# Optimization experiments

Hardware: AMD Instinct MI355X
Metric: run time of the kernel (lower is better)

## Reference

```python
import jax, jax.numpy as jnp
import numpy as np

TAU = 2.0
V_THRESHOLD = 1.0
V_RESET = 0.0

def setup_inputs() -> dict:
    key = jax.random.key(0)
    x = jax.random.normal(key, (4, 64, 262144), dtype=jnp.float32)
    return {"x": x}

def reference(x) -> jnp.ndarray:
    # MultiStepLIFNodePTT with decay_input=False, hard reset to v_reset=0.
    # Per step: v = v + x_t - (v - v_reset)/tau ; s = H(v - thresh) ; v = v*(1-s) + v_reset*s
    T = x.shape[0]
    flat = x.reshape(T, -1)  # [T, B*N]
    v0 = jnp.zeros_like(flat[0])

    def step(v, x_t):
        v = v + x_t - (v - V_RESET) * (1.0 / TAU)
        s = (v >= V_THRESHOLD).astype(v.dtype)
        v = v * (1.0 - s) + V_RESET * s
        return v, s

    _, spike_seq = jax.lax.scan(step, v0, flat)
    return spike_seq.reshape(x.shape)
```

## Files before the change

kernel.cpp:

```cpp
#include <hip/hip_runtime.h>


#define T_STEPS 4

typedef float vf4 __attribute__((ext_vector_type(4)));

__device__ __forceinline__ vf4 lif_step(vf4& v, const vf4 xt)
{
    v = 0.5f * v + xt;
    vf4 s;
    s.x = (v.x >= 1.0f) ? 1.0f : 0.0f;
    s.y = (v.y >= 1.0f) ? 1.0f : 0.0f;
    s.z = (v.z >= 1.0f) ? 1.0f : 0.0f;
    s.w = (v.w >= 1.0f) ? 1.0f : 0.0f;
    v.x = (v.x >= 1.0f) ? 0.0f : v.x;
    v.y = (v.y >= 1.0f) ? 0.0f : v.y;
    v.z = (v.z >= 1.0f) ? 0.0f : v.z;
    v.w = (v.w >= 1.0f) ? 0.0f : v.w;
    return s;
}

__global__ __launch_bounds__(256) void lif_spike_kernel(
    const vf4* __restrict__ x, vf4* __restrict__ out, unsigned n4)
{
    const unsigned S   = gridDim.x * blockDim.x;
    const unsigned tid = blockIdx.x * blockDim.x + threadIdx.x;

    if (tid + 3u * S < n4) {
        vf4 xv[4][T_STEPS];
#pragma unroll
        for (int k = 0; k < 4; ++k) {
            const unsigned i = tid + (unsigned)k * S;
#pragma unroll
            for (int t = 0; t < T_STEPS; ++t)
                xv[k][t] = __builtin_nontemporal_load(&x[(size_t)t * n4 + i]);
        }
#pragma unroll
        for (int k = 0; k < 4; ++k) {
            const unsigned i = tid + (unsigned)k * S;
            vf4 v = (vf4)(0.f);
#pragma unroll
            for (int t = 0; t < T_STEPS; ++t) {
                const vf4 s = lif_step(v, xv[k][t]);
                __builtin_nontemporal_store(s, &out[(size_t)t * n4 + i]);
            }
        }
    } else {
        for (unsigned i = tid; i < n4; i += S) {
            const vf4 x0 = __builtin_nontemporal_load(&x[(size_t)0 * n4 + i]);
            const vf4 x1 = __builtin_nontemporal_load(&x[(size_t)1 * n4 + i]);
            const vf4 x2 = __builtin_nontemporal_load(&x[(size_t)2 * n4 + i]);
            const vf4 x3 = __builtin_nontemporal_load(&x[(size_t)3 * n4 + i]);
            vf4 v = (vf4)(0.f);
            const vf4 s0 = lif_step(v, x0);
            const vf4 s1 = lif_step(v, x1);
            const vf4 s2 = lif_step(v, x2);
            const vf4 s3 = lif_step(v, x3);
            __builtin_nontemporal_store(s0, &out[(size_t)0 * n4 + i]);
            __builtin_nontemporal_store(s1, &out[(size_t)1 * n4 + i]);
            __builtin_nontemporal_store(s2, &out[(size_t)2 * n4 + i]);
            __builtin_nontemporal_store(s3, &out[(size_t)3 * n4 + i]);
        }
    }
}

extern "C" void kernel_launch(void* const* d_in, const int* in_sizes, int n_in,
                              void* d_out, int out_size, void* d_ws, size_t ws_size,
                              hipStream_t stream)
{
    const float* x = (const float*)d_in[0];
    float* out = (float*)d_out;

    const int n_total = in_sizes[0];
    const unsigned n4 = (unsigned)(n_total / T_STEPS / 4);

    const int block = 256;
    int grid = (int)(n4 / (unsigned)(block * 4));
    if (grid < 1) grid = 1;
    if ((unsigned)grid * (unsigned)block * 4u != n4) {
        grid = (int)((n4 + block - 1) / block);
        if (grid > 4096) grid = 4096;
    }

    lif_spike_kernel<<<grid, block, 0, stream>>>(
        (const vf4*)x, (vf4*)out, n4);
}
```

Before: 433.4 us.

## Simplify LIF kernel to fixed-grid grid-stride loop with regular stores

```diff
diff --git a/kernel.cpp b/kernel.cpp
--- a/kernel.cpp
+++ b/kernel.cpp
@@ -20,47 +20,26 @@
     return s;
 }
 
-__global__ __launch_bounds__(256) void lif_spike_kernel(
+__global__ __launch_bounds__(256, 8) void lif_spike_kernel(
     const vf4* __restrict__ x, vf4* __restrict__ out, unsigned n4)
 {
-    const unsigned S   = gridDim.x * blockDim.x;
-    const unsigned tid = blockIdx.x * blockDim.x + threadIdx.x;
+    const unsigned stride = gridDim.x * blockDim.x;
+    for (unsigned i = blockIdx.x * blockDim.x + threadIdx.x; i < n4; i += stride) {
+        const vf4 x0 = __builtin_nontemporal_load(&x[(size_t)0 * n4 + i]);
+        const vf4 x1 = __builtin_nontemporal_load(&x[(size_t)1 * n4 + i]);
+        const vf4 x2 = __builtin_nontemporal_load(&x[(size_t)2 * n4 + i]);
+        const vf4 x3 = __builtin_nontemporal_load(&x[(size_t)3 * n4 + i]);
 
-    if (tid + 3u * S < n4) {
-        vf4 xv[4][T_STEPS];
-#pragma unroll
-        for (int k = 0; k < 4; ++k) {
-            const unsigned i = tid + (unsigned)k * S;
-#pragma unroll
-            for (int t = 0; t < T_STEPS; ++t)
-                xv[k][t] = __builtin_nontemporal_load(&x[(size_t)t * n4 + i]);
-        }
-#pragma unroll
-        for (int k = 0; k < 4; ++k) {
-            const unsigned i = tid + (unsigned)k * S;
-            vf4 v = (vf4)(0.f);
-#pragma unroll
-            for (int t = 0; t < T_STEPS; ++t) {
-                const vf4 s = lif_step(v, xv[k][t]);
-                __builtin_nontemporal_store(s, &out[(size_t)t * n4 + i]);
-            }
-        }
-    } else {
-        for (unsigned i = tid; i < n4; i += S) {
-            const vf4 x0 = __builtin_nontemporal_load(&x[(size_t)0 * n4 + i]);
-            const vf4 x1 = __builtin_nontemporal_load(&x[(size_t)1 * n4 + i]);
-            const vf4 x2 = __builtin_nontemporal_load(&x[(size_t)2 * n4 + i]);
-            const vf4 x3 = __builtin_nontemporal_load(&x[(size_t)3 * n4 + i]);
-            vf4 v = (vf4)(0.f);
-            const vf4 s0 = lif_step(v, x0);
-            const vf4 s1 = lif_step(v, x1);
-            const vf4 s2 = lif_step(v, x2);
-            const vf4 s3 = lif_step(v, x3);
-            __builtin_nontemporal_store(s0, &out[(size_t)0 * n4 + i]);
-            __builtin_nontemporal_store(s1, &out[(size_t)1 * n4 + i]);
-            __builtin_nontemporal_store(s2, &out[(size_t)2 * n4 + i]);
-            __builtin_nontemporal_store(s3, &out[(size_t)3 * n4 + i]);
-        }
+        vf4 v = (vf4)(0.f);
+        const vf4 s0 = lif_step(v, x0);
+        const vf4 s1 = lif_step(v, x1);
+        const vf4 s2 = lif_step(v, x2);
+        const vf4 s3 = lif_step(v, x3);
+
+        out[(size_t)0 * n4 + i] = s0;
+        out[(size_t)1 * n4 + i] = s1;
+        out[(size_t)2 * n4 + i] = s2;
+        out[(size_t)3 * n4 + i] = s3;
     }
 }
 
@@ -75,12 +54,7 @@
     const unsigned n4 = (unsigned)(n_total / T_STEPS / 4);
 
     const int block = 256;
-    int grid = (int)(n4 / (unsigned)(block * 4));
-    if (grid < 1) grid = 1;
-    if ((unsigned)grid * (unsigned)block * 4u != n4) {
-        grid = (int)((n4 + block - 1) / block);
-        if (grid > 4096) grid = 4096;
-    }
+    const int grid = 4096;
 
     lif_spike_kernel<<<grid, block, 0, stream>>>(
         (const vf4*)x, (vf4*)out, n4);
```

Measured after the change: 431.4 us. No clear change (-0.5%).
